# Kernel optimization log

Measured on AMD Instinct MI355X. Metric: run time of the kernel, lower is better.

## Reference

```python
import jax, jax.numpy as jnp
import numpy as np

N = 100000  # num_nodes

def spmm(idx, val, x):
    # sparse [N,N] (COO: idx=[2,E], val=[E]) times dense x [N,F]
    rows, cols = idx[0], idx[1]
    return jax.ops.segment_sum(val[:, None] * x[cols], rows, num_segments=N)


def setup_inputs() -> dict:
    key = jax.random.key(0)
    ks = jax.random.split(key, 12)
    E = 3200000
    F_in, F_out = 128, 128
    inp = {
        "x": jax.random.normal(ks[0], (N, F_in), dtype=jnp.float32),
        "weight": jax.random.normal(ks[1], (F_in, F_out), dtype=jnp.float32) * (1.0 / np.sqrt(F_in)),
        "filter1": 0.9 + 0.2 * jax.random.uniform(ks[2], (N, 1), dtype=jnp.float32),
        "filter2": 0.9 + 0.2 * jax.random.uniform(ks[3], (N, 1), dtype=jnp.float32),
        "filter3": 0.9 + 0.2 * jax.random.uniform(ks[4], (N, 1), dtype=jnp.float32),
        "idx1": jax.random.randint(ks[5], (2, E), 0, N, dtype=jnp.int32),
        "val1": jax.random.normal(ks[6], (E,), dtype=jnp.float32) * 0.01,
        "idx2": jax.random.randint(ks[7], (2, E), 0, N, dtype=jnp.int32),
        "val2": jax.random.normal(ks[8], (E,), dtype=jnp.float32) * 0.01,
        "idx3": jax.random.randint(ks[9], (2, E), 0, N, dtype=jnp.int32),
        "val3": jax.random.normal(ks[10], (E,), dtype=jnp.float32) * 0.01,
    }
    return inp


def reference(x, weight, filter1, filter2, filter3, idx1, val1, idx2, val2, idx3, val3):
    # x = x @ W
    x = x @ weight
    # framelet transform: three spmm branches
    x1 = spmm(idx1, val1, x)
    x2 = spmm(idx2, val2, x)
    x3 = spmm(idx3, val3, x)
    # shrinkage is None -> no-op
    # elementwise learned filters
    x1 = filter1 * x1
    x2 = filter2 * x2
    x3 = filter3 * x3
    # inverse framelet transform
    x1 = spmm(idx1, val1, x1)
    x2 = spmm(idx2, val2, x2)
    x3 = spmm(idx3, val3, x3)
    return x1 + x2 + x3
```

## Files before the change

kernel.cpp:

```cpp
#include <hip/hip_runtime.h>
#include <hip/hip_bf16.h>


#define CHUNK 4096
#define CITER 16
#define MAXC 256

typedef __attribute__((ext_vector_type(8))) short short8;
typedef __attribute__((ext_vector_type(4))) float f32x4;
typedef __attribute__((ext_vector_type(4))) int int4v;

static __device__ __forceinline__ unsigned short bf16bits(float v) {
  return __builtin_bit_cast(unsigned short, __float2bfloat16(v));
}
static __device__ __forceinline__ float bflo(unsigned u) {
  return __uint_as_float(u << 16);
}
static __device__ __forceinline__ float bfhi(unsigned u) {
  return __uint_as_float(u & 0xffff0000u);
}

__global__ __launch_bounds__(256) void gemm_mfma(const float* __restrict__ x,
                                                 const float* __restrict__ w,
                                                 unsigned short* __restrict__ y,
                                                 int n) {
  __shared__ unsigned short wt[128][136];
  const int tid = threadIdx.x;
#pragma unroll
  for (int it = 0; it < 16; ++it) {
    int i = it * 256 + tid;
    int k = i >> 5;
    int c4 = (i & 31) << 2;
    float4 v = ((const float4*)w)[i];
    wt[c4 + 0][k] = bf16bits(v.x);
    wt[c4 + 1][k] = bf16bits(v.y);
    wt[c4 + 2][k] = bf16bits(v.z);
    wt[c4 + 3][k] = bf16bits(v.w);
  }
  __syncthreads();
  const int lane = tid & 63, wid = tid >> 6;
  const int lr = lane & 15, lq = lane >> 4;
  const int rowbase = blockIdx.x * 128 + wid * 32;
  f32x4 acc[2][8] = {};
#pragma unroll
  for (int ks = 0; ks < 4; ++ks) {
    short8 a[2];
#pragma unroll
    for (int s = 0; s < 2; ++s) {
      int r = rowbase + s * 16 + lr;
      float4 v0 = {0.f, 0.f, 0.f, 0.f}, v1 = {0.f, 0.f, 0.f, 0.f};
      if (r < n) {
        const float* xp = x + (size_t)r * 128 + ks * 32 + lq * 8;
        v0 = *(const float4*)xp;
        v1 = *(const float4*)(xp + 4);
      }
      a[s][0] = bf16bits(v0.x);
      a[s][1] = bf16bits(v0.y);
      a[s][2] = bf16bits(v0.z);
      a[s][3] = bf16bits(v0.w);
      a[s][4] = bf16bits(v1.x);
      a[s][5] = bf16bits(v1.y);
      a[s][6] = bf16bits(v1.z);
      a[s][7] = bf16bits(v1.w);
    }
#pragma unroll
    for (int cs = 0; cs < 8; ++cs) {
      short8 b = *(const short8*)&wt[cs * 16 + lr][ks * 32 + lq * 8];
      acc[0][cs] =
          __builtin_amdgcn_mfma_f32_16x16x32_bf16(a[0], b, acc[0][cs], 0, 0, 0);
      acc[1][cs] =
          __builtin_amdgcn_mfma_f32_16x16x32_bf16(a[1], b, acc[1][cs], 0, 0, 0);
    }
  }
#pragma unroll
  for (int s = 0; s < 2; ++s) {
#pragma unroll
    for (int cs = 0; cs < 8; ++cs) {
      int col = cs * 16 + lr;
      int r0 = rowbase + s * 16 + lq * 4;
#pragma unroll
      for (int j = 0; j < 4; ++j) {
        int r = r0 + j;
        if (r < n) y[(size_t)r * 128 + col] = bf16bits(acc[s][cs][j]);
      }
    }
  }
}

__global__ void ginit(int* __restrict__ gcur, int NC, int CAP) {
  int i = blockIdx.x * 256 + threadIdx.x;
  if (i < NC) gcur[i] = i * CAP;
}

__global__ __launch_bounds__(256) void scatter1(const int* __restrict__ rows,
                                                const int* __restrict__ cols,
                                                const float* __restrict__ vals,
                                                int* __restrict__ gcur,
                                                int2* __restrict__ st1, int E,
                                                int NC) {
  __shared__ int lh[MAXC], gb[MAXC], lc[MAXC];
  __shared__ int rc[CHUNK];
  const int tid = threadIdx.x;
  lh[tid] = 0;
  __syncthreads();
  const int base = blockIdx.x * CHUNK;
#pragma unroll
  for (int k = 0; k < CITER; ++k) {
    int e = base + k * 256 + tid;
    int r = -1;
    if (e < E) {
      r = __builtin_nontemporal_load(rows + e);
      atomicAdd(&lh[r >> 9], 1);
    }
    rc[k * 256 + tid] = r;
  }
  __syncthreads();
  if (tid < NC) {
    int n = lh[tid];
    gb[tid] = n ? atomicAdd(&gcur[tid], n) : 0;
    lc[tid] = 0;
  }
  __syncthreads();
#pragma unroll
  for (int k = 0; k < CITER; ++k) {
    int e = base + k * 256 + tid;
    int r = rc[k * 256 + tid];
    if (r >= 0) {
      int c = r >> 9;
      int off = atomicAdd(&lc[c], 1);
      int2 o;
      o.x = ((r & 511) << 17) | __builtin_nontemporal_load(cols + e);
      o.y = __float_as_int(__builtin_nontemporal_load(vals + e));
      st1[gb[c] + off] = o;
    }
  }
}

__global__ __launch_bounds__(512) void scatter2(const int* __restrict__ gcur,
                                                const int2* __restrict__ st1,
                                                int2* __restrict__ st2,
                                                int2* __restrict__ rowse,
                                                int CAP) {
  __shared__ int sh[512], cur[512];
  const int c = blockIdx.x, tid = threadIdx.x;
  const int a = c * CAP;
  const int b = gcur[c];
  sh[tid] = 0;
  __syncthreads();
  for (int e = a + tid; e < b; e += 512)
    atomicAdd(&sh[(st1[e].x >> 17) & 511], 1);
  __syncthreads();
  int v = sh[tid];
  __syncthreads();
  for (int o = 1; o < 512; o <<= 1) {
    int t2 = (tid >= o) ? sh[tid - o] : 0;
    __syncthreads();
    sh[tid] += t2;
    __syncthreads();
  }
  int end = a + sh[tid];
  int start = end - v;
  cur[tid] = start;
  rowse[c * 512 + tid] = make_int2(start, end);
  __syncthreads();
  for (int e = a + tid; e < b; e += 512) {
    int2 d = st1[e];
    int r = (d.x >> 17) & 511;
    int p = atomicAdd(&cur[r], 1);
    st2[p] = make_int2(d.x & 0x1FFFF, d.y);
  }
}

template <int MID>
__global__ __launch_bounds__(256) void spmm_w(
    const int2* __restrict__ rowse, const int2* __restrict__ edges,
    const unsigned short* __restrict__ src, unsigned short* __restrict__ dst,
    float* __restrict__ out, const float* __restrict__ filt, int N, int accm) {
  const int lane = threadIdx.x & 63, wid = threadIdx.x >> 6;
  const int row = blockIdx.x * 4 + wid;
  if (row >= N) return;
  const int2 se = rowse[row];
  int e = se.x;
  const int e1 = se.y;
  float a0 = 0.f, a1 = 0.f, b0 = 0.f, b1 = 0.f;
  const unsigned loff = (unsigned)(lane << 1);
  for (; e + 15 < e1; e += 16) {
    int4v p[8];
#pragma unroll
    for (int j = 0; j < 8; ++j)
      p[j] = __builtin_nontemporal_load((const int4v*)&edges[e + 2 * j]);
    unsigned u[16];
#pragma unroll
    for (int j = 0; j < 8; ++j) {
      u[2 * j] = *(const unsigned*)(src + (((size_t)p[j].x) << 7) + loff);
      u[2 * j + 1] = *(const unsigned*)(src + (((size_t)p[j].z) << 7) + loff);
    }
#pragma unroll
    for (int j = 0; j < 8; ++j) {
      float v0 = __int_as_float(p[j].y), v1 = __int_as_float(p[j].w);
      if (j & 1) {
        b0 += v0 * bflo(u[2 * j]);
        b1 += v0 * bfhi(u[2 * j]);
        b0 += v1 * bflo(u[2 * j + 1]);
        b1 += v1 * bfhi(u[2 * j + 1]);
      } else {
        a0 += v0 * bflo(u[2 * j]);
        a1 += v0 * bfhi(u[2 * j]);
        a0 += v1 * bflo(u[2 * j + 1]);
        a1 += v1 * bfhi(u[2 * j + 1]);
      }
    }
  }
  for (; e + 3 < e1; e += 4) {
    int4v pa = __builtin_nontemporal_load((const int4v*)&edges[e]);
    int4v pb = __builtin_nontemporal_load((const int4v*)&edges[e + 2]);
    unsigned u0 = *(const unsigned*)(src + (((size_t)pa.x) << 7) + loff);
    unsigned u1 = *(const unsigned*)(src + (((size_t)pa.z) << 7) + loff);
    unsigned u2 = *(const unsigned*)(src + (((size_t)pb.x) << 7) + loff);
    unsigned u3 = *(const unsigned*)(src + (((size_t)pb.z) << 7) + loff);
    float v0 = __int_as_float(pa.y), v1 = __int_as_float(pa.w);
    float v2 = __int_as_float(pb.y), v3 = __int_as_float(pb.w);
    a0 += v0 * bflo(u0);
    a1 += v0 * bfhi(u0);
    b0 += v1 * bflo(u1);
    b1 += v1 * bfhi(u1);
    a0 += v2 * bflo(u2);
    a1 += v2 * bfhi(u2);
    b0 += v3 * bflo(u3);
    b1 += v3 * bfhi(u3);
  }
  for (; e < e1; ++e) {
    int2 d = edges[e];
    unsigned u = *(const unsigned*)(src + (((size_t)d.x) << 7) + loff);
    float v = __int_as_float(d.y);
    a0 += v * bflo(u);
    a1 += v * bfhi(u);
  }
  a0 += b0;
  a1 += b1;
  if (MID) {
    float fl = filt[row];
    a0 *= fl;
    a1 *= fl;
    unsigned o = (unsigned)bf16bits(a0) | ((unsigned)bf16bits(a1) << 16);
    *(unsigned*)(dst + ((size_t)row << 7) + loff) = o;
  } else {
    float* op = out + ((size_t)row << 7) + loff;
    float2 r;
    r.x = a0;
    r.y = a1;
    if (accm) {
      float2 c = *(const float2*)op;
      r.x += c.x;
      r.y += c.y;
    }
    *(float2*)op = r;
  }
}

extern "C" void kernel_launch(void* const* d_in, const int* in_sizes, int n_in,
                              void* d_out, int out_size, void* d_ws, size_t ws_size,
                              hipStream_t stream) {
  const float* x = (const float*)d_in[0];
  const float* w = (const float*)d_in[1];
  const float* filt[3] = {(const float*)d_in[2], (const float*)d_in[3],
                          (const float*)d_in[4]};
  const int* idx[3] = {(const int*)d_in[5], (const int*)d_in[7],
                       (const int*)d_in[9]};
  const float* val[3] = {(const float*)d_in[6], (const float*)d_in[8],
                         (const float*)d_in[10]};
  const int N = in_sizes[2];
  const int E = in_sizes[6];
  float* out = (float*)d_out;

  const int NC = (N + 511) >> 9;
  const int CAP = (((E + NC - 1) / NC) + 4096 + 255) & ~255;

  char* ws = (char*)d_ws;
  const size_t NF16 = (size_t)N * 128 * sizeof(unsigned short);
  unsigned short* xW = (unsigned short*)ws;
  unsigned short* t = (unsigned short*)(ws + NF16);
  size_t off = 2 * NF16;
  int2* st1 = (int2*)(ws + off);
  off += (size_t)NC * CAP * 8;
  int2* st2 = (int2*)(ws + off);
  off += (size_t)NC * CAP * 8;
  int* gcur = (int*)(ws + off);
  off += (MAXC * 4 + 255) & ~(size_t)255;
  int2* rowse = (int2*)(ws + off);
  off += (size_t)(NC << 9) * 8;
  (void)ws_size;

  gemm_mfma<<<(N + 127) / 128, 256, 0, stream>>>(x, w, xW, N);

  const int gE = (E + CHUNK - 1) / CHUNK;
  const int gS = (N + 3) / 4;
  for (int b = 0; b < 3; ++b) {
    const int* rows = idx[b];
    const int* cols = idx[b] + E;
    ginit<<<(NC + 255) / 256, 256, 0, stream>>>(gcur, NC, CAP);
    scatter1<<<gE, 256, 0, stream>>>(rows, cols, val[b], gcur, st1, E, NC);
    scatter2<<<NC, 512, 0, stream>>>(gcur, st1, st2, rowse, CAP);
    spmm_w<1><<<gS, 256, 0, stream>>>(rowse, st2, xW, t, nullptr, filt[b], N, 0);
    spmm_w<0><<<gS, 256, 0, stream>>>(rowse, st2, t, nullptr, out, nullptr, N,
                                      b > 0 ? 1 : 0);
  }
}
```

Baseline: 1.066 ms.

## Fuse three inverse SpMMs into one kernel with per-branch CSR buffers

```diff
diff --git a/kernel.cpp b/kernel.cpp
--- a/kernel.cpp
+++ b/kernel.cpp
@@ -8,7 +8,6 @@
 
 typedef __attribute__((ext_vector_type(8))) short short8;
 typedef __attribute__((ext_vector_type(4))) float f32x4;
-typedef __attribute__((ext_vector_type(4))) int int4v;
 
 static __device__ __forceinline__ unsigned short bf16bits(float v) {
   return __builtin_bit_cast(unsigned short, __float2bfloat16(v));
@@ -171,6 +170,53 @@
   }
 }
 
+static __device__ __forceinline__ void row_dot(
+    int e, int e1, const int2* __restrict__ edges,
+    const unsigned short* __restrict__ src, unsigned loff, float& a0,
+    float& a1) {
+  for (; e + 7 < e1; e += 8) {
+    int4 p0 = *(const int4*)&edges[e];
+    int4 p1 = *(const int4*)&edges[e + 2];
+    int4 p2 = *(const int4*)&edges[e + 4];
+    int4 p3 = *(const int4*)&edges[e + 6];
+    unsigned u0 = *(const unsigned*)(src + (((size_t)p0.x) << 7) + loff);
+    unsigned u1 = *(const unsigned*)(src + (((size_t)p0.z) << 7) + loff);
+    unsigned u2 = *(const unsigned*)(src + (((size_t)p1.x) << 7) + loff);
+    unsigned u3 = *(const unsigned*)(src + (((size_t)p1.z) << 7) + loff);
+    unsigned u4 = *(const unsigned*)(src + (((size_t)p2.x) << 7) + loff);
+    unsigned u5 = *(const unsigned*)(src + (((size_t)p2.z) << 7) + loff);
+    unsigned u6 = *(const unsigned*)(src + (((size_t)p3.x) << 7) + loff);
+    unsigned u7 = *(const unsigned*)(src + (((size_t)p3.z) << 7) + loff);
+    float v0 = __int_as_float(p0.y), v1 = __int_as_float(p0.w);
+    float v2 = __int_as_float(p1.y), v3 = __int_as_float(p1.w);
+    float v4 = __int_as_float(p2.y), v5 = __int_as_float(p2.w);
+    float v6 = __int_as_float(p3.y), v7 = __int_as_float(p3.w);
+    a0 += v0 * bflo(u0);
+    a1 += v0 * bfhi(u0);
+    a0 += v1 * bflo(u1);
+    a1 += v1 * bfhi(u1);
+    a0 += v2 * bflo(u2);
+    a1 += v2 * bfhi(u2);
+    a0 += v3 * bflo(u3);
+    a1 += v3 * bfhi(u3);
+    a0 += v4 * bflo(u4);
+    a1 += v4 * bfhi(u4);
+    a0 += v5 * bflo(u5);
+    a1 += v5 * bfhi(u5);
+    a0 += v6 * bflo(u6);
+    a1 += v6 * bfhi(u6);
+    a0 += v7 * bflo(u7);
+    a1 += v7 * bfhi(u7);
+  }
+  for (; e < e1; ++e) {
+    int2 d = edges[e];
+    unsigned u = *(const unsigned*)(src + (((size_t)d.x) << 7) + loff);
+    float v = __int_as_float(d.y);
+    a0 += v * bflo(u);
+    a1 += v * bfhi(u);
+  }
+}
+
 template <int MID>
 __global__ __launch_bounds__(256) void spmm_w(
     const int2* __restrict__ rowse, const int2* __restrict__ edges,
@@ -180,64 +226,9 @@
   const int row = blockIdx.x * 4 + wid;
   if (row >= N) return;
   const int2 se = rowse[row];
-  int e = se.x;
-  const int e1 = se.y;
-  float a0 = 0.f, a1 = 0.f, b0 = 0.f, b1 = 0.f;
+  float a0 = 0.f, a1 = 0.f;
   const unsigned loff = (unsigned)(lane << 1);
-  for (; e + 15 < e1; e += 16) {
-    int4v p[8];
-#pragma unroll
-    for (int j = 0; j < 8; ++j)
-      p[j] = __builtin_nontemporal_load((const int4v*)&edges[e + 2 * j]);
-    unsigned u[16];
-#pragma unroll
-    for (int j = 0; j < 8; ++j) {
-      u[2 * j] = *(const unsigned*)(src + (((size_t)p[j].x) << 7) + loff);
-      u[2 * j + 1] = *(const unsigned*)(src + (((size_t)p[j].z) << 7) + loff);
-    }
-#pragma unroll
-    for (int j = 0; j < 8; ++j) {
-      float v0 = __int_as_float(p[j].y), v1 = __int_as_float(p[j].w);
-      if (j & 1) {
-        b0 += v0 * bflo(u[2 * j]);
-        b1 += v0 * bfhi(u[2 * j]);
-        b0 += v1 * bflo(u[2 * j + 1]);
-        b1 += v1 * bfhi(u[2 * j + 1]);
-      } else {
-        a0 += v0 * bflo(u[2 * j]);
-        a1 += v0 * bfhi(u[2 * j]);
-        a0 += v1 * bflo(u[2 * j + 1]);
-        a1 += v1 * bfhi(u[2 * j + 1]);
-      }
-    }
-  }
-  for (; e + 3 < e1; e += 4) {
-    int4v pa = __builtin_nontemporal_load((const int4v*)&edges[e]);
-    int4v pb = __builtin_nontemporal_load((const int4v*)&edges[e + 2]);
-    unsigned u0 = *(const unsigned*)(src + (((size_t)pa.x) << 7) + loff);
-    unsigned u1 = *(const unsigned*)(src + (((size_t)pa.z) << 7) + loff);
-    unsigned u2 = *(const unsigned*)(src + (((size_t)pb.x) << 7) + loff);
-    unsigned u3 = *(const unsigned*)(src + (((size_t)pb.z) << 7) + loff);
-    float v0 = __int_as_float(pa.y), v1 = __int_as_float(pa.w);
-    float v2 = __int_as_float(pb.y), v3 = __int_as_float(pb.w);
-    a0 += v0 * bflo(u0);
-    a1 += v0 * bfhi(u0);
-    b0 += v1 * bflo(u1);
-    b1 += v1 * bfhi(u1);
-    a0 += v2 * bflo(u2);
-    a1 += v2 * bfhi(u2);
-    b0 += v3 * bflo(u3);
-    b1 += v3 * bfhi(u3);
-  }
-  for (; e < e1; ++e) {
-    int2 d = edges[e];
-    unsigned u = *(const unsigned*)(src + (((size_t)d.x) << 7) + loff);
-    float v = __int_as_float(d.y);
-    a0 += v * bflo(u);
-    a1 += v * bfhi(u);
-  }
-  a0 += b0;
-  a1 += b1;
+  row_dot(se.x, se.y, edges, src, loff, a0, a1);
   if (MID) {
     float fl = filt[row];
     a0 *= fl;
@@ -258,6 +249,30 @@
   }
 }
 
+__global__ __launch_bounds__(256) void spmm_out3(
+    const int2* __restrict__ rs1, const int2* __restrict__ rs2,
+    const int2* __restrict__ rs3, const int2* __restrict__ e1,
+    const int2* __restrict__ e2, const int2* __restrict__ e3,
+    const unsigned short* __restrict__ t1, const unsigned short* __restrict__ t2,
+    const unsigned short* __restrict__ t3, float* __restrict__ out, int N) {
+  const int lane = threadIdx.x & 63, wid = threadIdx.x >> 6;
+  const int row = blockIdx.x * 4 + wid;
+  if (row >= N) return;
+  float a0 = 0.f, a1 = 0.f;
+  const unsigned loff = (unsigned)(lane << 1);
+  int2 s;
+  s = rs1[row];
+  row_dot(s.x, s.y, e1, t1, loff, a0, a1);
+  s = rs2[row];
+  row_dot(s.x, s.y, e2, t2, loff, a0, a1);
+  s = rs3[row];
+  row_dot(s.x, s.y, e3, t3, loff, a0, a1);
+  float2 r;
+  r.x = a0;
+  r.y = a1;
+  *(float2*)(out + ((size_t)row << 7) + loff) = r;
+}
+
 extern "C" void kernel_launch(void* const* d_in, const int* in_sizes, int n_in,
                               void* d_out, int out_size, void* d_ws, size_t ws_size,
                               hipStream_t stream) {
@@ -274,35 +289,74 @@
   float* out = (float*)d_out;
 
   const int NC = (N + 511) >> 9;
-  const int CAP = (((E + NC - 1) / NC) + 4096 + 255) & ~255;
+  const int CAP = (((E + NC - 1) / NC) + 2048 + 255) & ~255;
+  const size_t NF16 = (size_t)N * 128 * sizeof(unsigned short);
+  const size_t STB = (size_t)NC * CAP * 8;
+  const size_t RSB = ((size_t)(NC << 9) * 8 + 255) & ~(size_t)255;
+  const size_t GCB = (MAXC * 4 + 255) & ~(size_t)255;
+
+  const size_t need_fused = 4 * NF16 + 4 * STB + 3 * RSB + GCB;
+  const bool fused = (ws_size >= need_fused);
 
   char* ws = (char*)d_ws;
-  const size_t NF16 = (size_t)N * 128 * sizeof(unsigned short);
-  unsigned short* xW = (unsigned short*)ws;
-  unsigned short* t = (unsigned short*)(ws + NF16);
-  size_t off = 2 * NF16;
-  int2* st1 = (int2*)(ws + off);
-  off += (size_t)NC * CAP * 8;
-  int2* st2 = (int2*)(ws + off);
-  off += (size_t)NC * CAP * 8;
-  int* gcur = (int*)(ws + off);
-  off += (MAXC * 4 + 255) & ~(size_t)255;
-  int2* rowse = (int2*)(ws + off);
-  off += (size_t)(NC << 9) * 8;
-  (void)ws_size;
-
-  gemm_mfma<<<(N + 127) / 128, 256, 0, stream>>>(x, w, xW, N);
-
   const int gE = (E + CHUNK - 1) / CHUNK;
   const int gS = (N + 3) / 4;
-  for (int b = 0; b < 3; ++b) {
-    const int* rows = idx[b];
-    const int* cols = idx[b] + E;
-    ginit<<<(NC + 255) / 256, 256, 0, stream>>>(gcur, NC, CAP);
-    scatter1<<<gE, 256, 0, stream>>>(rows, cols, val[b], gcur, st1, E, NC);
-    scatter2<<<NC, 512, 0, stream>>>(gcur, st1, st2, rowse, CAP);
-    spmm_w<1><<<gS, 256, 0, stream>>>(rowse, st2, xW, t, nullptr, filt[b], N, 0);
-    spmm_w<0><<<gS, 256, 0, stream>>>(rowse, st2, t, nullptr, out, nullptr, N,
-                                      b > 0 ? 1 : 0);
-  }
-}
+
+  if (fused) {
+    unsigned short* xW = (unsigned short*)ws;
+    unsigned short* t[3];
+    t[0] = (unsigned short*)(ws + NF16);
+    t[1] = (unsigned short*)(ws + 2 * NF16);
+    t[2] = (unsigned short*)(ws + 3 * NF16);
+    size_t off = 4 * NF16;
+    int2* st1 = (int2*)(ws + off);
+    off += STB;
+    int2* st2[3];
+    for (int b = 0; b < 3; ++b) {
+      st2[b] = (int2*)(ws + off);
+      off += STB;
+    }
+    int2* rowse[3];
+    for (int b = 0; b < 3; ++b) {
+      rowse[b] = (int2*)(ws + off);
+      off += RSB;
+    }
+    int* gcur = (int*)(ws + off);
+
+    gemm_mfma<<<(N + 127) / 128, 256, 0, stream>>>(x, w, xW, N);
+    for (int b = 0; b < 3; ++b) {
+      ginit<<<(NC + 255) / 256, 256, 0, stream>>>(gcur, NC, CAP);
+      scatter1<<<gE, 256, 0, stream>>>(idx[b], idx[b] + E, val[b], gcur, st1,
+                                       E, NC);
+      scatter2<<<NC, 512, 0, stream>>>(gcur, st1, st2[b], rowse[b], CAP);
+    }
+    for (int b = 0; b < 3; ++b)
+      spmm_w<1><<<gS, 256, 0, stream>>>(rowse[b], st2[b], xW, t[b], nullptr,
+                                        filt[b], N, 0);
+    spmm_out3<<<gS, 256, 0, stream>>>(rowse[0], rowse[1], rowse[2], st2[0],
+                                      st2[1], st2[2], t[0], t[1], t[2], out, N);
+  } else {
+    unsigned short* xW = (unsigned short*)ws;
+    unsigned short* t = (unsigned short*)(ws + NF16);
+    size_t off = 2 * NF16;
+    int2* st1 = (int2*)(ws + off);
+    off += STB;
+    int2* st2 = (int2*)(ws + off);
+    off += STB;
+    int2* rowse = (int2*)(ws + off);
+    off += RSB;
+    int* gcur = (int*)(ws + off);
+
+    gemm_mfma<<<(N + 127) / 128, 256, 0, stream>>>(x, w, xW, N);
+    for (int b = 0; b < 3; ++b) {
+      ginit<<<(NC + 255) / 256, 256, 0, stream>>>(gcur, NC, CAP);
+      scatter1<<<gE, 256, 0, stream>>>(idx[b], idx[b] + E, val[b], gcur, st1,
+                                       E, NC);
+      scatter2<<<NC, 512, 0, stream>>>(gcur, st1, st2, rowse, CAP);
+      spmm_w<1><<<gS, 256, 0, stream>>>(rowse, st2, xW, t, nullptr, filt[b], N,
+                                        0);
+      spmm_w<0><<<gS, 256, 0, stream>>>(rowse, st2, t, nullptr, out, nullptr,
+                                        N, b > 0 ? 1 : 0);
+    }
+  }
+}
```

Result: faster. 1.027 ms (-3.7%).
